# Kernel optimization log

Hardware: AMD Instinct MI355X
Metric: run time of the kernel (lower is better)

The kernel has to match this reference:

```python
import jax, jax.numpy as jnp
import numpy as np

KH = KW = 5  # receptive field


def _pair_w(a, b):
    # a, b: [...] in [0,1] -> soft one-hot over the 2-bit address (a = high bit): [..., 4]
    sa = jnp.stack([1.0 - a, a], axis=-1)
    sb = jnp.stack([1.0 - b, b], axis=-1)
    return (sa[..., :, None] * sb[..., None, :]).reshape(*a.shape, 4)


def _lut_nodes(g, lut):
    # g: [N, T, M, 6] node inputs in [0,1]; lut: [T, M, 64] raw LUT params.
    # DWN-style differentiable LUT: out = sum_a sigmoid(lut[a]) * prod_j (x_j if bit_j else 1-x_j)
    T, M = lut.shape[0], lut.shape[1]
    p = jax.nn.sigmoid(lut).reshape(T, M, 4, 4, 4)  # bits grouped pairwise, MSB-first
    Wa = _pair_w(g[..., 0], g[..., 1])  # [N,T,M,4]
    Wb = _pair_w(g[..., 2], g[..., 3])
    Wc = _pair_w(g[..., 4], g[..., 5])
    return jnp.einsum('tmpqr,ntmp,ntmq,ntmr->ntm', p, Wa, Wb, Wc)


def _lut_layer(h, idx, lut):
    # h: [N, T, P] previous-layer activations per tree; idx: [T, M, 6] in [0,P)
    T = idx.shape[0]
    g = h[:, jnp.arange(T)[:, None, None], idx]  # gather: [N, T, M, 6]
    return _lut_nodes(g, lut)


def setup_inputs() -> dict:
    key = jax.random.key(0)
    ks = jax.random.split(key, 7)
    x = jax.random.uniform(ks[0], (64, 1, 8, 8), dtype=jnp.float32)
    idx0 = jax.random.randint(ks[1], (128, 36, 6), 0, 25, dtype=jnp.int32)
    lut0 = jax.random.normal(ks[2], (128, 36, 64), dtype=jnp.float32)
    idx1 = jax.random.randint(ks[3], (128, 6, 6), 0, 36, dtype=jnp.int32)
    lut1 = jax.random.normal(ks[4], (128, 6, 64), dtype=jnp.float32)
    idx2 = jax.random.randint(ks[5], (128, 1, 6), 0, 6, dtype=jnp.int32)
    lut2 = jax.random.normal(ks[6], (128, 1, 64), dtype=jnp.float32)
    return dict(x=x, idx0=idx0, lut0=lut0, idx1=idx1, lut1=lut1, idx2=idx2, lut2=lut2)


def reference(x, idx0, lut0, idx1, lut1, idx2, lut2):
    B, C, H, W = x.shape
    oh, ow = H - KH + 1, W - KW + 1  # stride 1, padding 0 (as in nn.Unfold here)
    # im2col unfold, channel-major then (kh, kw) -- matches nn.Unfold ordering
    patches = jnp.stack(
        [x[:, c, i:i + oh, j:j + ow] for c in range(C) for i in range(KH) for j in range(KW)],
        axis=1,
    )  # [B, C*KH*KW, oh, ow]
    feat = patches.reshape(B, C * KH * KW, oh * ow).transpose(0, 2, 1).reshape(-1, C * KH * KW)  # [N, 25]
    # layer 0: gather from shared patch features into every tree
    g0 = feat[:, idx0]                      # [N, T, 36, 6]
    h0 = _lut_nodes(g0, lut0)               # [N, T, 36]
    h1 = _lut_layer(h0, idx1, lut1)         # [N, T, 6]
    h2 = _lut_layer(h1, idx2, lut2)         # [N, T, 1]
    T = lut0.shape[0]
    out = h2[..., 0].reshape(B, oh * ow, T).transpose(0, 2, 1).reshape(B, T, oh, ow)
    return out
```

## Files before the change

kernel.cpp:

```cpp
#include <hip/hip_runtime.h>

#define T_TREES 128
#define M0 36
#define M1 6
#define NROWS 1024
#define XPAD 67

typedef float v2f __attribute__((ext_vector_type(2)));

__device__ __forceinline__ float sigmoidf(float v) {
    return 1.f / (1.f + __expf(-v));
}

__device__ __forceinline__ void pair_w(v2f a, v2f b, v2f w[4]) {
    v2f ab = a * b;
    w[3] = ab;
    w[2] = a - ab;
    w[1] = b - ab;
    w[0] = (1.f - a) - w[1];
}

__device__ __forceinline__ v2f lut_node_v2(const float* __restrict__ P,
                                           v2f a, v2f b, v2f c,
                                           v2f d, v2f e, v2f f) {
    v2f wa[4], wb[4], wc[4];
    pair_w(a, b, wa);
    pair_w(c, d, wb);
    pair_w(e, f, wc);
    v2f acc = {0.f, 0.f};
#pragma unroll
    for (int p = 0; p < 4; ++p) {
        v2f tp = {0.f, 0.f};
#pragma unroll
        for (int q = 0; q < 4; ++q) {
            const float* Pq = P + p * 16 + q * 4;
            v2f tq = Pq[0] * wc[0] + Pq[1] * wc[1] + Pq[2] * wc[2] + Pq[3] * wc[3];
            tp += tq * wb[q];
        }
        acc += tp * wa[p];
    }
    return acc;
}

__global__ __launch_bounds__(256, 1) void l0_kernel(
    const float* __restrict__ x, const int* __restrict__ idx0,
    const float* __restrict__ lut0, float* __restrict__ h0) {
    __shared__ float xs[64 * XPAD];
    __shared__ __align__(16) float Ps[4 * 64];

    const int tid = threadIdx.x;
    const int bx = blockIdx.x;
    const int t = bx & 127;
    const int mg = bx >> 7;

#pragma unroll
    for (int k = 0; k < 4; ++k) {
        int i4 = tid + k * 256;
        float4 v = reinterpret_cast<const float4*>(x)[i4];
        float* dst = xs + (i4 >> 4) * XPAD + (i4 & 15) * 4;
        dst[0] = v.x; dst[1] = v.y; dst[2] = v.z; dst[3] = v.w;
    }
    Ps[tid] = sigmoidf(lut0[(t * M0 + mg * 4) * 64 + tid]);
    __syncthreads();

    const int w = tid >> 6, ln = tid & 63;
    const int m = mg * 4 + w;

    float P[64];
#pragma unroll
    for (int i = 0; i < 16; ++i) {
        float4 v = reinterpret_cast<const float4*>(Ps + w * 64)[i];
        P[4 * i] = v.x; P[4 * i + 1] = v.y; P[4 * i + 2] = v.z; P[4 * i + 3] = v.w;
    }

    const int* id = idx0 + (t * M0 + m) * 6;
    int di[6];
#pragma unroll
    for (int j = 0; j < 6; ++j) {
        int k = id[j];
        int ii = (k * 13) >> 6;
        di[j] = k - 5 * ii + ii * 8;
    }

    float* __restrict__ hout = h0 + (t * M0 + m) * NROWS;
#pragma unroll 2
    for (int u = 0; u < 8; ++u) {
        int p = u * 64 + ln;
        int b = p >> 3;
        int s = (p & 7) * 2;
        int xb = b * XPAD + (s >> 2) * 8 + (s & 3);
        v2f g[6];
#pragma unroll
        for (int j = 0; j < 6; ++j) {
            int a0 = xb + di[j];
            g[j].x = xs[a0];
            g[j].y = xs[a0 + 1];
        }
        v2f r = lut_node_v2(P, g[0], g[1], g[2], g[3], g[4], g[5]);
        *reinterpret_cast<v2f*>(hout + 2 * p) = r;
    }
}

__global__ __launch_bounds__(384) void l12_kernel(
    const float* __restrict__ h0, const int* __restrict__ idx1,
    const float* __restrict__ lut1, const int* __restrict__ idx2,
    const float* __restrict__ lut2, float* __restrict__ out) {
    __shared__ __align__(16) float Ps[(M1 + 1) * 64];
    __shared__ __align__(8) float h1s[M1 * 256];

    const int tid = threadIdx.x;
    const int bx = blockIdx.x;
    const int t = bx & 127;
    const int q = bx >> 7;

    for (int i = tid; i < (M1 + 1) * 64; i += 384) {
        float v = (i < M1 * 64) ? lut1[t * (M1 * 64) + i] : lut2[t * 64 + (i - M1 * 64)];
        Ps[i] = sigmoidf(v);
    }
    __syncthreads();

    const int w = tid >> 6, ln = tid & 63;

    {
        float P[64];
#pragma unroll
        for (int i = 0; i < 16; ++i) {
            float4 v = reinterpret_cast<const float4*>(Ps + w * 64)[i];
            P[4 * i] = v.x; P[4 * i + 1] = v.y; P[4 * i + 2] = v.z; P[4 * i + 3] = v.w;
        }
        const int* id = idx1 + (t * M1 + w) * 6;
        const float* c0 = h0 + (t * M0 + id[0]) * NROWS;
        const float* c1 = h0 + (t * M0 + id[1]) * NROWS;
        const float* c2 = h0 + (t * M0 + id[2]) * NROWS;
        const float* c3 = h0 + (t * M0 + id[3]) * NROWS;
        const float* c4 = h0 + (t * M0 + id[4]) * NROWS;
        const float* c5 = h0 + (t * M0 + id[5]) * NROWS;
#pragma unroll
        for (int u = 0; u < 2; ++u) {
            int pl = u * 64 + ln;
            int rr = q * 256 + 2 * pl;
            v2f r = lut_node_v2(P,
                *reinterpret_cast<const v2f*>(c0 + rr),
                *reinterpret_cast<const v2f*>(c1 + rr),
                *reinterpret_cast<const v2f*>(c2 + rr),
                *reinterpret_cast<const v2f*>(c3 + rr),
                *reinterpret_cast<const v2f*>(c4 + rr),
                *reinterpret_cast<const v2f*>(c5 + rr));
            *reinterpret_cast<v2f*>(h1s + w * 256 + 2 * pl) = r;
        }
    }
    __syncthreads();

    if (tid < 128) {
        float P[64];
#pragma unroll
        for (int i = 0; i < 16; ++i) {
            float4 v = reinterpret_cast<const float4*>(Ps + M1 * 64)[i];
            P[4 * i] = v.x; P[4 * i + 1] = v.y; P[4 * i + 2] = v.z; P[4 * i + 3] = v.w;
        }
        const int* id = idx2 + t * 6;
        int rl = 2 * tid;
        v2f r = lut_node_v2(P,
            *reinterpret_cast<const v2f*>(h1s + id[0] * 256 + rl),
            *reinterpret_cast<const v2f*>(h1s + id[1] * 256 + rl),
            *reinterpret_cast<const v2f*>(h1s + id[2] * 256 + rl),
            *reinterpret_cast<const v2f*>(h1s + id[3] * 256 + rl),
            *reinterpret_cast<const v2f*>(h1s + id[4] * 256 + rl),
            *reinterpret_cast<const v2f*>(h1s + id[5] * 256 + rl));
        int row = q * 256 + rl;
        int b = row >> 4, s = row & 15;
        *reinterpret_cast<v2f*>(out + b * (T_TREES * 16) + t * 16 + s) = r;
    }
}

__global__ __launch_bounds__(128) void clut_fb_kernel(
    const float* __restrict__ x,
    const int* __restrict__ idx0, const float* __restrict__ lut0,
    const int* __restrict__ idx1, const float* __restrict__ lut1,
    const int* __restrict__ idx2, const float* __restrict__ lut2,
    float* __restrict__ out) {
    __shared__ __align__(16) float slut[43 * 64];
    __shared__ float feat[25 * 128];
    __shared__ float h0[M0 * 128];
    __shared__ float h1[M1 * 128];

    const int tid = threadIdx.x;
    const int t = blockIdx.y;
    for (int i = tid; i < 43 * 64; i += 128) {
        float v;
        if (i < M0 * 64)              v = lut0[t * (M0 * 64) + i];
        else if (i < (M0 + M1) * 64)  v = lut1[t * (M1 * 64) + (i - M0 * 64)];
        else                          v = lut2[t * 64 + (i - (M0 + M1) * 64)];
        slut[i] = sigmoidf(v);
    }
    const int n = blockIdx.x * 128 + tid;
    const int b = n >> 4, s = n & 15;
    const float* xb = x + b * 64 + (s >> 2) * 8 + (s & 3);
#pragma unroll
    for (int i = 0; i < 5; ++i)
#pragma unroll
        for (int j = 0; j < 5; ++j)
            feat[(i * 5 + j) * 128 + tid] = xb[i * 8 + j];
    __syncthreads();
    for (int m = 0; m < M0; ++m) {
        const int* id = idx0 + (t * M0 + m) * 6;
        v2f g[6];
#pragma unroll
        for (int j = 0; j < 6; ++j) { g[j].x = feat[id[j] * 128 + tid]; g[j].y = 0.f; }
        v2f r = lut_node_v2(slut + m * 64, g[0], g[1], g[2], g[3], g[4], g[5]);
        h0[m * 128 + tid] = r.x;
    }
    for (int m = 0; m < M1; ++m) {
        const int* id = idx1 + (t * M1 + m) * 6;
        v2f g[6];
#pragma unroll
        for (int j = 0; j < 6; ++j) { g[j].x = h0[id[j] * 128 + tid]; g[j].y = 0.f; }
        v2f r = lut_node_v2(slut + (M0 + m) * 64, g[0], g[1], g[2], g[3], g[4], g[5]);
        h1[m * 128 + tid] = r.x;
    }
    {
        const int* id = idx2 + t * 6;
        v2f g[6];
#pragma unroll
        for (int j = 0; j < 6; ++j) { g[j].x = h1[id[j] * 128 + tid]; g[j].y = 0.f; }
        v2f r = lut_node_v2(slut + (M0 + M1) * 64, g[0], g[1], g[2], g[3], g[4], g[5]);
        out[b * (T_TREES * 16) + t * 16 + s] = r.x;
    }
}

extern "C" void kernel_launch(void* const* d_in, const int* in_sizes, int n_in,
                              void* d_out, int out_size, void* d_ws, size_t ws_size,
                              hipStream_t stream) {
    const float* x    = (const float*)d_in[0];
    const int*   idx0 = (const int*)  d_in[1];
    const float* lut0 = (const float*)d_in[2];
    const int*   idx1 = (const int*)  d_in[3];
    const float* lut1 = (const float*)d_in[4];
    const int*   idx2 = (const int*)  d_in[5];
    const float* lut2 = (const float*)d_in[6];
    float* out = (float*)d_out;

    const size_t h0_bytes = (size_t)T_TREES * M0 * NROWS * sizeof(float);
    if (ws_size >= h0_bytes) {
        float* h0 = (float*)d_ws;
        l0_kernel<<<dim3((M0 / 4) * T_TREES), 256, 0, stream>>>(x, idx0, lut0, h0);
        l12_kernel<<<dim3(4 * T_TREES), 384, 0, stream>>>(h0, idx1, lut1, idx2, lut2, out);
    } else {
        dim3 grid(NROWS / 128, T_TREES);
        clut_fb_kernel<<<grid, 128, 0, stream>>>(x, idx0, lut0, idx1, lut1, idx2, lut2, out);
    }
}
```

Before: 24.63 us.

## Fuse all three LUT layers into one kernel keeping h0 in shared memory

Replaces the two-kernel path (layer 0 writing h0 to global workspace, then layers 1-2 reading it back) with a single kernel per (tree, row-quarter) block. The block computes all 36 layer-0 nodes for its 256 rows into shared memory, then layers 1 and 2. This removes the global round trip of the h0 buffer and one kernel launch. In exchange, each block recomputes sigmoid over all 43 LUT tables and the full x tile, and uses about 64KB of LDS, which may limit occupancy.

```diff
diff --git a/kernel.cpp b/kernel.cpp
--- a/kernel.cpp
+++ b/kernel.cpp
@@ -3,7 +3,7 @@
 #define T_TREES 128
 #define M0 36
 #define M1 6
-#define NROWS 1024
+#define NNODES 43
 #define XPAD 67
 
 typedef float v2f __attribute__((ext_vector_type(2)));
@@ -42,70 +42,15 @@
     return acc;
 }
 
-__global__ __launch_bounds__(256, 1) void l0_kernel(
-    const float* __restrict__ x, const int* __restrict__ idx0,
-    const float* __restrict__ lut0, float* __restrict__ h0) {
+__global__ __launch_bounds__(384, 3) void fused_kernel(
+    const float* __restrict__ x,
+    const int* __restrict__ idx0, const float* __restrict__ lut0,
+    const int* __restrict__ idx1, const float* __restrict__ lut1,
+    const int* __restrict__ idx2, const float* __restrict__ lut2,
+    float* __restrict__ out) {
     __shared__ float xs[64 * XPAD];
-    __shared__ __align__(16) float Ps[4 * 64];
-
-    const int tid = threadIdx.x;
-    const int bx = blockIdx.x;
-    const int t = bx & 127;
-    const int mg = bx >> 7;
-
-#pragma unroll
-    for (int k = 0; k < 4; ++k) {
-        int i4 = tid + k * 256;
-        float4 v = reinterpret_cast<const float4*>(x)[i4];
-        float* dst = xs + (i4 >> 4) * XPAD + (i4 & 15) * 4;
-        dst[0] = v.x; dst[1] = v.y; dst[2] = v.z; dst[3] = v.w;
-    }
-    Ps[tid] = sigmoidf(lut0[(t * M0 + mg * 4) * 64 + tid]);
-    __syncthreads();
-
-    const int w = tid >> 6, ln = tid & 63;
-    const int m = mg * 4 + w;
-
-    float P[64];
-#pragma unroll
-    for (int i = 0; i < 16; ++i) {
-        float4 v = reinterpret_cast<const float4*>(Ps + w * 64)[i];
-        P[4 * i] = v.x; P[4 * i + 1] = v.y; P[4 * i + 2] = v.z; P[4 * i + 3] = v.w;
-    }
-
-    const int* id = idx0 + (t * M0 + m) * 6;
-    int di[6];
-#pragma unroll
-    for (int j = 0; j < 6; ++j) {
-        int k = id[j];
-        int ii = (k * 13) >> 6;
-        di[j] = k - 5 * ii + ii * 8;
-    }
-
-    float* __restrict__ hout = h0 + (t * M0 + m) * NROWS;
-#pragma unroll 2
-    for (int u = 0; u < 8; ++u) {
-        int p = u * 64 + ln;
-        int b = p >> 3;
-        int s = (p & 7) * 2;
-        int xb = b * XPAD + (s >> 2) * 8 + (s & 3);
-        v2f g[6];
-#pragma unroll
-        for (int j = 0; j < 6; ++j) {
-            int a0 = xb + di[j];
-            g[j].x = xs[a0];
-            g[j].y = xs[a0 + 1];
-        }
-        v2f r = lut_node_v2(P, g[0], g[1], g[2], g[3], g[4], g[5]);
-        *reinterpret_cast<v2f*>(hout + 2 * p) = r;
-    }
-}
-
-__global__ __launch_bounds__(384) void l12_kernel(
-    const float* __restrict__ h0, const int* __restrict__ idx1,
-    const float* __restrict__ lut1, const int* __restrict__ idx2,
-    const float* __restrict__ lut2, float* __restrict__ out) {
-    __shared__ __align__(16) float Ps[(M1 + 1) * 64];
+    __shared__ __align__(16) float Ps[NNODES * 64];
+    __shared__ __align__(8) float h0s[M0 * 256];
     __shared__ __align__(8) float h1s[M1 * 256];
 
     const int tid = threadIdx.x;
@@ -113,40 +58,74 @@
     const int t = bx & 127;
     const int q = bx >> 7;
 
-    for (int i = tid; i < (M1 + 1) * 64; i += 384) {
-        float v = (i < M1 * 64) ? lut1[t * (M1 * 64) + i] : lut2[t * 64 + (i - M1 * 64)];
+    for (int i = tid; i < 4096; i += 384)
+        xs[(i >> 6) * XPAD + (i & 63)] = x[i];
+    for (int i = tid; i < NNODES * 64; i += 384) {
+        float v;
+        if (i < M0 * 64)              v = lut0[t * (M0 * 64) + i];
+        else if (i < (M0 + M1) * 64)  v = lut1[t * (M1 * 64) + (i - M0 * 64)];
+        else                          v = lut2[t * 64 + (i - (M0 + M1) * 64)];
         Ps[i] = sigmoidf(v);
     }
     __syncthreads();
 
     const int w = tid >> 6, ln = tid & 63;
 
+#pragma unroll 1
+    for (int k = 0; k < 6; ++k) {
+        const int m = w * 6 + k;
+        float P[64];
+#pragma unroll
+        for (int i = 0; i < 16; ++i) {
+            float4 v = reinterpret_cast<const float4*>(Ps + m * 64)[i];
+            P[4 * i] = v.x; P[4 * i + 1] = v.y; P[4 * i + 2] = v.z; P[4 * i + 3] = v.w;
+        }
+        const int* id = idx0 + (t * M0 + m) * 6;
+        int di[6];
+#pragma unroll
+        for (int j = 0; j < 6; ++j) {
+            int kk = id[j];
+            int ii = (kk * 13) >> 6;
+            di[j] = kk - 5 * ii + ii * 8;
+        }
+#pragma unroll
+        for (int u = 0; u < 2; ++u) {
+            int pl = u * 64 + ln;
+            int r = 2 * pl;
+            int row = q * 256 + r;
+            int b = row >> 4, s = row & 15;
+            int xb = b * XPAD + (s >> 2) * 8 + (s & 3);
+            v2f g[6];
+#pragma unroll
+            for (int j = 0; j < 6; ++j) {
+                int a0 = xb + di[j];
+                g[j].x = xs[a0];
+                g[j].y = xs[a0 + 1];
+            }
+            v2f rr = lut_node_v2(P, g[0], g[1], g[2], g[3], g[4], g[5]);
+            *reinterpret_cast<v2f*>(h0s + m * 256 + r) = rr;
+        }
+    }
+    __syncthreads();
+
     {
         float P[64];
 #pragma unroll
         for (int i = 0; i < 16; ++i) {
-            float4 v = reinterpret_cast<const float4*>(Ps + w * 64)[i];
+            float4 v = reinterpret_cast<const float4*>(Ps + (M0 + w) * 64)[i];
             P[4 * i] = v.x; P[4 * i + 1] = v.y; P[4 * i + 2] = v.z; P[4 * i + 3] = v.w;
         }
         const int* id = idx1 + (t * M1 + w) * 6;
-        const float* c0 = h0 + (t * M0 + id[0]) * NROWS;
-        const float* c1 = h0 + (t * M0 + id[1]) * NROWS;
-        const float* c2 = h0 + (t * M0 + id[2]) * NROWS;
-        const float* c3 = h0 + (t * M0 + id[3]) * NROWS;
-        const float* c4 = h0 + (t * M0 + id[4]) * NROWS;
-        const float* c5 = h0 + (t * M0 + id[5]) * NROWS;
 #pragma unroll
         for (int u = 0; u < 2; ++u) {
             int pl = u * 64 + ln;
-            int rr = q * 256 + 2 * pl;
-            v2f r = lut_node_v2(P,
-                *reinterpret_cast<const v2f*>(c0 + rr),
-                *reinterpret_cast<const v2f*>(c1 + rr),
-                *reinterpret_cast<const v2f*>(c2 + rr),
-                *reinterpret_cast<const v2f*>(c3 + rr),
-                *reinterpret_cast<const v2f*>(c4 + rr),
-                *reinterpret_cast<const v2f*>(c5 + rr));
-            *reinterpret_cast<v2f*>(h1s + w * 256 + 2 * pl) = r;
+            int r = 2 * pl;
+            v2f g[6];
+#pragma unroll
+            for (int j = 0; j < 6; ++j)
+                g[j] = *reinterpret_cast<const v2f*>(h0s + id[j] * 256 + r);
+            v2f rr = lut_node_v2(P, g[0], g[1], g[2], g[3], g[4], g[5]);
+            *reinterpret_cast<v2f*>(h1s + w * 256 + r) = rr;
         }
     }
     __syncthreads();
@@ -155,76 +134,19 @@
         float P[64];
 #pragma unroll
         for (int i = 0; i < 16; ++i) {
-            float4 v = reinterpret_cast<const float4*>(Ps + M1 * 64)[i];
+            float4 v = reinterpret_cast<const float4*>(Ps + (M0 + M1) * 64)[i];
             P[4 * i] = v.x; P[4 * i + 1] = v.y; P[4 * i + 2] = v.z; P[4 * i + 3] = v.w;
         }
         const int* id = idx2 + t * 6;
-        int rl = 2 * tid;
-        v2f r = lut_node_v2(P,
-            *reinterpret_cast<const v2f*>(h1s + id[0] * 256 + rl),
-            *reinterpret_cast<const v2f*>(h1s + id[1] * 256 + rl),
-            *reinterpret_cast<const v2f*>(h1s + id[2] * 256 + rl),
-            *reinterpret_cast<const v2f*>(h1s + id[3] * 256 + rl),
-            *reinterpret_cast<const v2f*>(h1s + id[4] * 256 + rl),
-            *reinterpret_cast<const v2f*>(h1s + id[5] * 256 + rl));
-        int row = q * 256 + rl;
-        int b = row >> 4, s = row & 15;
-        *reinterpret_cast<v2f*>(out + b * (T_TREES * 16) + t * 16 + s) = r;
-    }
-}
-
-__global__ __launch_bounds__(128) void clut_fb_kernel(
-    const float* __restrict__ x,
-    const int* __restrict__ idx0, const float* __restrict__ lut0,
-    const int* __restrict__ idx1, const float* __restrict__ lut1,
-    const int* __restrict__ idx2, const float* __restrict__ lut2,
-    float* __restrict__ out) {
-    __shared__ __align__(16) float slut[43 * 64];
-    __shared__ float feat[25 * 128];
-    __shared__ float h0[M0 * 128];
-    __shared__ float h1[M1 * 128];
-
-    const int tid = threadIdx.x;
-    const int t = blockIdx.y;
-    for (int i = tid; i < 43 * 64; i += 128) {
-        float v;
-        if (i < M0 * 64)              v = lut0[t * (M0 * 64) + i];
-        else if (i < (M0 + M1) * 64)  v = lut1[t * (M1 * 64) + (i - M0 * 64)];
-        else                          v = lut2[t * 64 + (i - (M0 + M1) * 64)];
-        slut[i] = sigmoidf(v);
-    }
-    const int n = blockIdx.x * 128 + tid;
-    const int b = n >> 4, s = n & 15;
-    const float* xb = x + b * 64 + (s >> 2) * 8 + (s & 3);
-#pragma unroll
-    for (int i = 0; i < 5; ++i)
-#pragma unroll
-        for (int j = 0; j < 5; ++j)
-            feat[(i * 5 + j) * 128 + tid] = xb[i * 8 + j];
-    __syncthreads();
-    for (int m = 0; m < M0; ++m) {
-        const int* id = idx0 + (t * M0 + m) * 6;
+        int r = 2 * tid;
         v2f g[6];
 #pragma unroll
-        for (int j = 0; j < 6; ++j) { g[j].x = feat[id[j] * 128 + tid]; g[j].y = 0.f; }
-        v2f r = lut_node_v2(slut + m * 64, g[0], g[1], g[2], g[3], g[4], g[5]);
-        h0[m * 128 + tid] = r.x;
-    }
-    for (int m = 0; m < M1; ++m) {
-        const int* id = idx1 + (t * M1 + m) * 6;
-        v2f g[6];
-#pragma unroll
-        for (int j = 0; j < 6; ++j) { g[j].x = h0[id[j] * 128 + tid]; g[j].y = 0.f; }
-        v2f r = lut_node_v2(slut + (M0 + m) * 64, g[0], g[1], g[2], g[3], g[4], g[5]);
-        h1[m * 128 + tid] = r.x;
-    }
-    {
-        const int* id = idx2 + t * 6;
-        v2f g[6];
-#pragma unroll
-        for (int j = 0; j < 6; ++j) { g[j].x = h1[id[j] * 128 + tid]; g[j].y = 0.f; }
-        v2f r = lut_node_v2(slut + (M0 + M1) * 64, g[0], g[1], g[2], g[3], g[4], g[5]);
-        out[b * (T_TREES * 16) + t * 16 + s] = r.x;
+        for (int j = 0; j < 6; ++j)
+            g[j] = *reinterpret_cast<const v2f*>(h1s + id[j] * 256 + r);
+        v2f o = lut_node_v2(P, g[0], g[1], g[2], g[3], g[4], g[5]);
+        int row = q * 256 + r;
+        int b = row >> 4, s = row & 15;
+        *reinterpret_cast<v2f*>(out + b * (T_TREES * 16) + t * 16 + s) = o;
     }
 }
 
@@ -240,13 +162,6 @@
     const float* lut2 = (const float*)d_in[6];
     float* out = (float*)d_out;
 
-    const size_t h0_bytes = (size_t)T_TREES * M0 * NROWS * sizeof(float);
-    if (ws_size >= h0_bytes) {
-        float* h0 = (float*)d_ws;
-        l0_kernel<<<dim3((M0 / 4) * T_TREES), 256, 0, stream>>>(x, idx0, lut0, h0);
-        l12_kernel<<<dim3(4 * T_TREES), 384, 0, stream>>>(h0, idx1, lut1, idx2, lut2, out);
-    } else {
-        dim3 grid(NROWS / 128, T_TREES);
-        clut_fb_kernel<<<grid, 128, 0, stream>>>(x, idx0, lut0, idx1, lut1, idx2, lut2, out);
-    }
+    fused_kernel<<<dim3(4 * T_TREES), 384, 0, stream>>>(
+        x, idx0, lut0, idx1, lut1, idx2, lut2, out);
 }
```

Result: slower. 27.27 us (+10.7%).
